# Kernel tuning notes

Measured on AMD Instinct MI355X. Metric: run time of the kernel, lower is better.

## Reference

```python
import jax, jax.numpy as jnp
import numpy as np

NUM_HEADS = 12
NUM_FRAMES = 8
WINDOW = (14, 14)


def _gen_relative_position_index(ws):
    h, w = ws
    num_rel = (2 * h - 1) * (2 * w - 1) + 3
    area = h * w
    coords = np.stack(np.meshgrid(np.arange(h), np.arange(w), indexing='ij'))  # (2,h,w)
    cf = coords.reshape(2, -1)
    rel = cf[:, :, None] - cf[:, None, :]  # (2,A,A)
    rel = rel.transpose(1, 2, 0).astype(np.int64)
    rel[:, :, 0] += h - 1
    rel[:, :, 1] += w - 1
    rel[:, :, 0] *= 2 * w - 1
    idx = np.zeros((area + 1, area + 1), dtype=np.int32)
    idx[1:, 1:] = rel.sum(-1)
    idx[0, :] = num_rel - 3
    idx[:, 0] = num_rel - 2
    idx[0, 0] = num_rel - 1
    return idx


def _gen_relative_temporal_index(nf):
    c = np.arange(nf)
    return (c[:, None] - c[None, :] + nf - 1).astype(np.int32)


def setup_inputs() -> dict:
    key = jax.random.key(0)
    ks = jax.random.split(key, 8)
    B, N, C = 2, NUM_FRAMES * WINDOW[0] * WINDOW[1], 768  # N = 1568
    num_rel = (2 * WINDOW[0] - 1) * (2 * WINDOW[1] - 1) + 3  # 732
    return {
        'x': jax.random.normal(ks[0], (B, N, C), jnp.float32),
        'qkv_w': jax.random.normal(ks[1], (3 * C, C), jnp.float32) * 0.02,
        'q_bias': jax.random.normal(ks[2], (C,), jnp.float32) * 0.02,
        'v_bias': jax.random.normal(ks[3], (C,), jnp.float32) * 0.02,
        'rel_pos_table': jax.random.normal(ks[4], (num_rel, NUM_HEADS), jnp.float32) * 0.02,
        'rel_temp_table': jax.random.normal(ks[5], (2 * NUM_FRAMES - 1, NUM_HEADS), jnp.float32) * 0.02,
        'proj_w': jax.random.normal(ks[6], (C, C), jnp.float32) * 0.02,
        'proj_b': jax.random.normal(ks[7], (C,), jnp.float32) * 0.02,
        'rel_pos_index': jnp.asarray(_gen_relative_position_index(WINDOW)),
        'rel_temp_index': jnp.asarray(_gen_relative_temporal_index(NUM_FRAMES)),
    }


def reference(x, qkv_w, q_bias, v_bias, rel_pos_table, rel_temp_table, proj_w, proj_b,
              rel_pos_index, rel_temp_index):
    B, N, C = x.shape
    H = NUM_HEADS
    D = C // H
    scale = D ** -0.5
    nf = NUM_FRAMES

    # qkv projection with concat(q_bias, zeros(k), v_bias)
    qkv_bias = jnp.concatenate([q_bias, jnp.zeros_like(q_bias), v_bias])
    qkv = x @ qkv_w.T + qkv_bias  # [B,N,3C]
    qkv = qkv.reshape(B, N, 3, H, D).transpose(2, 0, 3, 1, 4)  # [3,B,H,N,D]
    q, k, v = qkv[0], qkv[1], qkv[2]

    attn = jnp.einsum('bhqd,bhkd->bhqk', q * scale, k)  # [B,H,N,N]

    # gathered 2D relative position bias, tiled over frames, sliced to N
    rel = rel_pos_table[rel_pos_index]  # [197,197,H]
    rel = jnp.transpose(rel, (2, 0, 1))[None]  # [1,H,197,197]
    rel = jnp.tile(rel, (1, 1, nf, nf))[:, :, :N, :N]
    attn = attn + rel

    # temporal bias, repeat_interleave by tokens-per-frame
    tpf = N // nf  # 196
    temp = rel_temp_table[rel_temp_index]  # [nf,nf,H]
    temp = jnp.transpose(temp, (2, 0, 1))[None]  # [1,H,nf,nf]
    temp = jnp.repeat(jnp.repeat(temp, tpf, axis=2), tpf, axis=3)  # [1,H,N,N]
    attn = attn + temp

    attn = jax.nn.softmax(attn, axis=-1)
    attn = jnp.nan_to_num(attn, nan=0.0)

    out = jnp.einsum('bhqk,bhkd->bhqd', attn, v)  # [B,H,N,D]
    out = out.transpose(0, 2, 1, 3).reshape(B, N, C)
    return out @ proj_w.T + proj_b
```

## Files before the change

### kernel.cpp

```cpp
#include <hip/hip_runtime.h>
#include <hip/hip_bf16.h>

#define NHEADS 12
#define NFRAMES 8
#define NTOK 1568
#define CDIM 768
#define DHEAD 64
#define BATCH 2
#define MROWS (BATCH * NTOK)
#define MPAD 3200
#define K3 (3 * CDIM)
#define AREA1 197
#define TPF 196
#define LOG2E 1.4426950408889634f

typedef __bf16 bf16x8 __attribute__((ext_vector_type(8)));
typedef float f32x4 __attribute__((ext_vector_type(4)));
typedef float f32x16 __attribute__((ext_vector_type(16)));
typedef unsigned short u16x8 __attribute__((ext_vector_type(8)));

#if __has_builtin(__builtin_amdgcn_exp2f)
#define EXP2(x) __builtin_amdgcn_exp2f(x)
#else
#define EXP2(x) exp2f(x)
#endif

__device__ __forceinline__ unsigned short f2bf(float f) {
  return __builtin_bit_cast(unsigned short, (__bf16)f);
}
__device__ __forceinline__ float bf2f(unsigned short u) {
  unsigned int x = ((unsigned int)u) << 16;
  return __builtin_bit_cast(float, x);
}
__device__ __forceinline__ bf16x8 ld8(const unsigned short* p) {
  return __builtin_bit_cast(bf16x8, *(const u16x8*)p);
}
__device__ __forceinline__ f32x4 mfma16(bf16x8 a, bf16x8 b, f32x4 c) {
  return __builtin_amdgcn_mfma_f32_16x16x32_bf16(a, b, c, 0, 0, 0);
}
__device__ __forceinline__ f32x16 mfma32(bf16x8 a, bf16x8 b, f32x16 c) {
  return __builtin_amdgcn_mfma_f32_32x32x16_bf16(a, b, c, 0, 0, 0);
}
__device__ __forceinline__ unsigned int pack2(float lo, float hi) {
  return ((unsigned int)f2bf(hi) << 16) | (unsigned int)f2bf(lo);
}
__device__ __forceinline__ void swap32(unsigned int a, unsigned int b,
                                       unsigned int& x, unsigned int& y) {
#if __has_builtin(__builtin_amdgcn_permlane32_swap)
  auto r = __builtin_amdgcn_permlane32_swap(a, b, false, false);
  x = r[0]; y = r[1];
#else
  const bool hi = (threadIdx.x & 63) >= 32;
  unsigned int ea = (unsigned int)__shfl_xor((int)a, 32);
  unsigned int eb = (unsigned int)__shfl_xor((int)b, 32);
  x = hi ? eb : a;
  y = hi ? b : ea;
#endif
}
#define GL_LDS(src, dst)                                                    \
  __builtin_amdgcn_global_load_lds(                                         \
      (const __attribute__((address_space(1))) void*)(src),                 \
      (__attribute__((address_space(3))) void*)(dst), 16, 0, 0)

__device__ __forceinline__ int xcd_swz(int lin, int nwg) {
  const int q = nwg >> 3, r = nwg & 7;
  const int xcd = lin & 7, idx = lin >> 3;
  return (xcd < r ? xcd * (q + 1) : r * (q + 1) + (xcd - r) * q) + idx;
}

__global__ void biasP_kernel(const float* __restrict__ rpt,
                             const int* __restrict__ rpi,
                             const float* __restrict__ rtt,
                             const int* __restrict__ rti,
                             unsigned short* __restrict__ biasP,
                             float* __restrict__ bias2) {
  if (blockIdx.x == NHEADS * AREA1) {
    int t = threadIdx.x;
    for (; t < NHEADS * 64; t += 256) {
      int h = t >> 6, ff = t & 63;
      bias2[t] = rtt[rti[ff] * NHEADS + h] * LOG2E;
    }
    return;
  }
  __shared__ float row[AREA1];
  const int h = blockIdx.x / AREA1;
  const int i = blockIdx.x - h * AREA1;
  for (int j = threadIdx.x; j < AREA1; j += 256)
    row[j] = rpt[rpi[i * AREA1 + j] * NHEADS + h] * LOG2E;
  __syncthreads();
  unsigned short* dst = biasP + (size_t)blockIdx.x * 49 * 32;
  for (int e = threadIdx.x; e < 49 * 32; e += 256) {
    const int t = e >> 5, r = e & 31;
    const int hi = r >> 4, rr = r & 15;
    int km = 32 * t + (rr & 3) + 8 * (rr >> 2) + 4 * hi;
    km %= AREA1;
    dst[e] = f2bf(row[km]);
  }
}

template <int MODE, int BM, int BN, int TPB, int WAVES_M, int NB_N>
__global__ __launch_bounds__(TPB) void gemm_kernel(
    const float* __restrict__ Afp,
    const unsigned short* __restrict__ Abf,
    const float* __restrict__ Bfp,
    const float* __restrict__ bias0,
    const float* __restrict__ biasv,
    unsigned short* __restrict__ qbuf,
    unsigned short* __restrict__ kbuf,
    unsigned short* __restrict__ vtbuf,
    float* __restrict__ Cout) {
  constexpr int WAVES = TPB / 64;
  constexpr int WAVES_N = WAVES / WAVES_M;
  constexpr int WM = BM / WAVES_M;
  constexpr int WN = BN / WAVES_N;
  static_assert(BM * 4 == TPB && BN * 4 == TPB, "one chunk per thread");
  __shared__ unsigned short As[2][BM * 32];
  __shared__ unsigned short Bs[2][BN * 32];
  const int lane = threadIdx.x & 63;
  const int wv = threadIdx.x >> 6;
  const int tid = threadIdx.x;
  const int wg = xcd_swz(blockIdx.x, gridDim.x);
  const int m0 = (wg / NB_N) * BM;
  const int n0 = (wg % NB_N) * BN;

  const int srow = tid >> 2;
  const int srcc = (tid & 3) ^ ((tid >> 3) & 3);
  int arow = m0 + srow; if (arow >= MROWS) arow = MROWS - 1;
  const int brow = n0 + srow;

  f32x4 ra0, ra1, rb0, rb1;
  auto issueLoads = [&](int kt, int buf) {
    const int k0 = kt * 32 + srcc * 8;
    if (MODE == 0) {
      const f32x4* ap = (const f32x4*)(Afp + (size_t)arow * CDIM + k0);
      ra0 = ap[0]; ra1 = ap[1];
    } else {
      GL_LDS(Abf + (size_t)arow * CDIM + k0, &As[buf][tid * 8]);
    }
    const f32x4* bp = (const f32x4*)(Bfp + (size_t)brow * CDIM + k0);
    rb0 = bp[0]; rb1 = bp[1];
  };
  auto writeStage = [&](int buf) {
    u16x8 w;
    if (MODE == 0) {
      w[0] = f2bf(ra0[0]); w[1] = f2bf(ra0[1]); w[2] = f2bf(ra0[2]);
      w[3] = f2bf(ra0[3]); w[4] = f2bf(ra1[0]); w[5] = f2bf(ra1[1]);
      w[6] = f2bf(ra1[2]); w[7] = f2bf(ra1[3]);
      *(u16x8*)&As[buf][tid * 8] = w;
    }
    w[0] = f2bf(rb0[0]); w[1] = f2bf(rb0[1]); w[2] = f2bf(rb0[2]);
    w[3] = f2bf(rb0[3]); w[4] = f2bf(rb1[0]); w[5] = f2bf(rb1[1]);
    w[6] = f2bf(rb1[2]); w[7] = f2bf(rb1[3]);
    *(u16x8*)&Bs[buf][tid * 8] = w;
  };

  f32x4 acc[WM / 16][WN / 16] = {};
  const int rbase = (wv & (WAVES_M - 1)) * WM;
  const int cbase = (wv / WAVES_M) * WN;
  const int lc = lane >> 4;

  issueLoads(0, 0);
  __builtin_amdgcn_sched_barrier(0);
  writeStage(0);
  __syncthreads();
  int cur = 0;
  for (int kt = 0; kt < CDIM / 32; ++kt) {
    if (kt + 1 < CDIM / 32) issueLoads(kt + 1, cur ^ 1);
    __builtin_amdgcn_sched_barrier(0);
    bf16x8 af[WM / 16], bg[WN / 16];
#pragma unroll
    for (int i = 0; i < WM / 16; ++i) {
      const int ra = rbase + i * 16 + (lane & 15);
      af[i] = ld8(&As[cur][ra * 32 + ((lc ^ ((ra >> 1) & 3)) << 3)]);
    }
#pragma unroll
    for (int j = 0; j < WN / 16; ++j) {
      const int rb = cbase + j * 16 + (lane & 15);
      bg[j] = ld8(&Bs[cur][rb * 32 + ((lc ^ ((rb >> 1) & 3)) << 3)]);
    }
#pragma unroll
    for (int i = 0; i < WM / 16; ++i)
#pragma unroll
      for (int j = 0; j < WN / 16; ++j)
        acc[i][j] = mfma16(af[i], bg[j], acc[i][j]);
    if (kt + 1 < CDIM / 32) writeStage(cur ^ 1);
    __syncthreads();
    cur ^= 1;
  }

#pragma unroll
  for (int i = 0; i < WM / 16; ++i) {
#pragma unroll
    for (int j = 0; j < WN / 16; ++j) {
#pragma unroll
      for (int r = 0; r < 4; ++r) {
        int grow = m0 + rbase + i * 16 + (lane >> 4) * 4 + r;
        int gcol = n0 + cbase + j * 16 + (lane & 15);
        if (grow >= MROWS) continue;
        float v = acc[i][j][r];
        if (MODE == 0) {
          int which = gcol / CDIM;
          int cc = gcol - which * CDIM;
          int hh = cc >> 6, dd = cc & 63;
          int b = grow / NTOK, n = grow - b * NTOK;
          size_t hd = ((size_t)(b * NHEADS + hh) * NTOK + n) * 64 + dd;
          if (which == 0)
            qbuf[hd] = f2bf((v + bias0[cc]) * (0.125f * LOG2E));
          else if (which == 1)
            kbuf[hd] = f2bf(v);
          else
            vtbuf[((size_t)(b * NHEADS + hh) * 64 + dd) * NTOK + n] =
                f2bf(v + biasv[cc]);
        } else {
          Cout[(size_t)grow * CDIM + gcol] = v + bias0[gcol];
        }
      }
    }
  }
}

__global__ __launch_bounds__(256) void attn_kernel(
    const unsigned short* __restrict__ qbuf,
    const unsigned short* __restrict__ kbuf,
    const unsigned short* __restrict__ vtbuf,
    const unsigned short* __restrict__ biasP,
    const float* __restrict__ bias2,
    unsigned short* __restrict__ aout) {
  __shared__ __align__(16) char smem[36864];
  unsigned short* stg = (unsigned short*)smem;
  float* mb = (float*)smem;

  const int lane = threadIdx.x & 63;
  const int wv = threadIdx.x >> 6;
  const int wu = (blockIdx.x & 7) * 147 + (blockIdx.x >> 3);
  const int bh = wu / 49;
  const int qt = wu - bh * 49;
  const int q0 = qt * 32;
  const int h = bh % NHEADS;
  const int b = bh / NHEADS;
  const int qlane = lane & 31;
  const int hi = lane >> 5;
  const int hi4 = hi * 4;
  const int qn = q0 + qlane;
  const int qfr = qn / TPF < 7 ? qn / TPF : 7;
  const int qmod = qn % AREA1;

  const unsigned short* qp = qbuf + (size_t)bh * NTOK * DHEAD;
  const unsigned short* kp = kbuf + (size_t)bh * NTOK * DHEAD;
  const unsigned short* vp = vtbuf + (size_t)bh * DHEAD * NTOK;
  const unsigned short* bP = biasP + ((size_t)(h * AREA1 + qmod) * 49) * 32 + hi * 16;
  const float* b2q = bias2 + h * 64 + qfr * 8;

  unsigned short* KsW = stg + wv * 4096;
  unsigned short* VsW = KsW + 2048;

  const unsigned short* ksb =
      kp + (size_t)(lane >> 3) * DHEAD + (((lane & 7) ^ (lane >> 3)) << 3);
  const unsigned short* vsb =
      vp + (size_t)(lane >> 2) * NTOK + (((lane & 3) ^ ((lane >> 3) & 3)) << 3);

  auto stage = [&](int gt) {
    const int kv0 = gt * 32;
#pragma unroll
    for (int j = 0; j < 4; ++j) {
      GL_LDS(ksb + (size_t)(kv0 + j * 8) * DHEAD, KsW + j * 512);
      GL_LDS(vsb + kv0 + (size_t)(j * 16) * NTOK, VsW + j * 512);
    }
  };

  bf16x8 aq[4];
#pragma unroll
  for (int c = 0; c < 4; ++c)
    aq[c] = ld8(qp + (size_t)qn * DHEAD + c * 16 + hi * 8);

  f32x16 o0 = {}, o1 = {};
  float lrun = 0.f;

  stage(wv);
  u16x8 ubA, ubB;
  {
    const u16x8* bp = (const u16x8*)(bP + (size_t)wv * 32);
    ubA = bp[0]; ubB = bp[1];
  }
  int kfl = 0;
  float b2lo = b2q[0], b2hi = b2q[1];
  const int skey = qlane & 7;
  const int vswz = (qlane >> 1) & 3;

  for (int gt = wv; gt < 49; gt += 4) {
    asm volatile("s_waitcnt vmcnt(0)" ::: "memory");
    __builtin_amdgcn_sched_barrier(0);
    bf16x8 kf[4];
#pragma unroll
    for (int c = 0; c < 4; ++c)
      kf[c] = ld8(&KsW[qlane * 64 + ((((c << 1) + hi) ^ skey) << 3)]);
    bf16x8 vf0 = ld8(&VsW[qlane * 32 + ((hi ^ vswz) << 3)]);
    bf16x8 vf1 = ld8(&VsW[qlane * 32 + (((2 + hi) ^ vswz) << 3)]);
    bf16x8 vf2 = ld8(&VsW[(32 + qlane) * 32 + ((hi ^ vswz) << 3)]);
    bf16x8 vf3 = ld8(&VsW[(32 + qlane) * 32 + (((2 + hi) ^ vswz) << 3)]);
    asm volatile("s_waitcnt lgkmcnt(0)" ::: "memory");
    __builtin_amdgcn_sched_barrier(0);
    const bool more = (gt + 4 < 49);
    if (more) stage(gt + 4);

    f32x16 s;
#pragma unroll
    for (int r = 0; r < 16; ++r)
      s[r] = ((r < 8) ? bf2f(ubA[r]) : bf2f(ubB[r - 8])) + b2lo;
    __builtin_amdgcn_s_setprio(1);
#pragma unroll
    for (int c = 0; c < 4; ++c) s = mfma32(kf[c], aq[c], s);
    __builtin_amdgcn_s_setprio(0);

    const int ccr = (kfl + 1) * TPF - gt * 32;
    int kfln = kfl;
    float nb2lo = b2lo, nb2hi = b2hi;
    if (more) {
      const u16x8* bp = (const u16x8*)(bP + (size_t)(gt + 4) * 32);
      ubA = bp[0]; ubB = bp[1];
      kfln = ((gt + 4) * 8) / 49;
      nb2lo = b2q[kfln];
      nb2hi = b2q[kfln < 7 ? kfln + 1 : 7];
    }

    if (ccr < 32) {
      const float dlt = b2hi - b2lo;
#pragma unroll
      for (int r = 0; r < 16; ++r)
        s[r] += ((r & 3) + 8 * (r >> 2) + hi4 >= ccr) ? dlt : 0.f;
    }

#pragma unroll
    for (int r = 0; r < 16; ++r) s[r] = EXP2(s[r]);
    float ps;
    {
      float a = (s[0] + s[1]) + (s[2] + s[3]);
      float bb = (s[4] + s[5]) + (s[6] + s[7]);
      float cc = (s[8] + s[9]) + (s[10] + s[11]);
      float dd = (s[12] + s[13]) + (s[14] + s[15]);
      ps = (a + bb) + (cc + dd);
    }
    {
      unsigned int px, py;
      swap32(__builtin_bit_cast(unsigned int, ps),
             __builtin_bit_cast(unsigned int, ps), px, py);
      ps = __builtin_bit_cast(float, px) + __builtin_bit_cast(float, py);
    }
    lrun += ps;

    unsigned int dw[8];
#pragma unroll
    for (int c = 0; c < 8; ++c) dw[c] = pack2(s[2 * c], s[2 * c + 1]);
    unsigned int f0[4], f1[4];
    swap32(dw[0], dw[2], f0[0], f0[2]);
    swap32(dw[1], dw[3], f0[1], f0[3]);
    swap32(dw[4], dw[6], f1[0], f1[2]);
    swap32(dw[5], dw[7], f1[1], f1[3]);
    const bf16x8 F0 = __builtin_bit_cast(bf16x8, *(ulonglong2*)f0);
    const bf16x8 F1 = __builtin_bit_cast(bf16x8, *(ulonglong2*)f1);

    __builtin_amdgcn_s_setprio(1);
    o0 = mfma32(vf0, F0, o0);
    o0 = mfma32(vf1, F1, o0);
    o1 = mfma32(vf2, F0, o1);
    o1 = mfma32(vf3, F1, o1);
    __builtin_amdgcn_s_setprio(0);

    kfl = kfln;
    b2lo = nb2lo;
    b2hi = nb2hi;
  }

  __syncthreads();
  float* mrow = mb + (size_t)(wv * 64 + lane) * 34;
#pragma unroll
  for (int r = 0; r < 16; ++r) {
    mrow[r] = o0[r];
    mrow[16 + r] = o1[r];
  }
  mrow[32] = lrun;
  __syncthreads();
  if (wv < 2) {
    const int off = wv * 16;
    float acc[16];
#pragma unroll
    for (int r = 0; r < 16; ++r) acc[r] = 0.f;
    float L = 0.f;
#pragma unroll
    for (int w2 = 0; w2 < 4; ++w2) {
      const float* rr = mb + (size_t)(w2 * 64 + lane) * 34;
      L += rr[32];
#pragma unroll
      for (int r = 0; r < 16; ++r) acc[r] += rr[off + r];
    }
    const float rinv = 1.0f / L;
    unsigned short* op = aout + (size_t)(b * NTOK + qn) * CDIM + h * 64 + wv * 32;
#pragma unroll
    for (int c = 0; c < 8; ++c) {
      const int d0 = 8 * (c >> 1) + 4 * hi + 2 * (c & 1);
      *(unsigned int*)(op + d0) = pack2(acc[2 * c] * rinv, acc[2 * c + 1] * rinv);
    }
  }
}

extern "C" void kernel_launch(void* const* d_in, const int* in_sizes, int n_in,
                              void* d_out, int out_size, void* d_ws, size_t ws_size,
                              hipStream_t stream) {
  (void)in_sizes; (void)n_in; (void)out_size; (void)ws_size;
  const float* x        = (const float*)d_in[0];
  const float* qkv_w    = (const float*)d_in[1];
  const float* q_bias   = (const float*)d_in[2];
  const float* v_bias   = (const float*)d_in[3];
  const float* rp_table = (const float*)d_in[4];
  const float* rt_table = (const float*)d_in[5];
  const float* proj_w   = (const float*)d_in[6];
  const float* proj_b   = (const float*)d_in[7];
  const int* rp_index   = (const int*)d_in[8];
  const int* rt_index   = (const int*)d_in[9];

  char* ws = (char*)d_ws;
  unsigned short* qbuf   = (unsigned short*)(ws + 9633792);
  unsigned short* kbuf   = (unsigned short*)(ws + 14450688);
  unsigned short* vtbuf  = (unsigned short*)(ws + 19267584);
  unsigned short* aout   = (unsigned short*)(ws + 24084480);
  unsigned short* biasP  = (unsigned short*)(ws);
  float* bias2           = (float*)(ws + 30247424);

  gemm_kernel<0, 128, 128, 512, 4, K3 / 128>
      <<<dim3((K3 / 128) * (MPAD / 128)), 512, 0, stream>>>(
          x, nullptr, qkv_w, q_bias, v_bias, qbuf, kbuf, vtbuf, nullptr);
  biasP_kernel<<<NHEADS * AREA1 + 1, 256, 0, stream>>>(
      rp_table, rp_index, rt_table, rt_index, biasP, bias2);
  attn_kernel<<<dim3(1176), 256, 0, stream>>>(
      qbuf, kbuf, vtbuf, biasP, bias2, aout);
  gemm_kernel<1, 64, 64, 256, 2, CDIM / 64>
      <<<dim3((CDIM / 64) * (MPAD / 64)), 256, 0, stream>>>(
          nullptr, aout, proj_w, proj_b, nullptr, nullptr, nullptr, nullptr,
          (float*)d_out);
}
```

Before: 113.6 us.

## Fuse relative-bias table build into a dedicated QKV projection GEMM kernel

```diff
diff --git a/kernel.cpp b/kernel.cpp
--- a/kernel.cpp
+++ b/kernel.cpp
@@ -68,33 +68,148 @@
   return (xcd < r ? xcd * (q + 1) : r * (q + 1) + (xcd - r) * q) + idx;
 }
 
-__global__ void biasP_kernel(const float* __restrict__ rpt,
-                             const int* __restrict__ rpi,
-                             const float* __restrict__ rtt,
-                             const int* __restrict__ rti,
-                             unsigned short* __restrict__ biasP,
-                             float* __restrict__ bias2) {
-  if (blockIdx.x == NHEADS * AREA1) {
-    int t = threadIdx.x;
-    for (; t < NHEADS * 64; t += 256) {
-      int h = t >> 6, ff = t & 63;
-      bias2[t] = rtt[rti[ff] * NHEADS + h] * LOG2E;
+__global__ __launch_bounds__(512) void gemm0_kernel(
+    const float* __restrict__ x,
+    const float* __restrict__ qkv_w,
+    const float* __restrict__ q_bias,
+    const float* __restrict__ v_bias,
+    unsigned short* __restrict__ qbuf,
+    unsigned short* __restrict__ kbuf,
+    unsigned short* __restrict__ vtbuf,
+    const float* __restrict__ rpt,
+    const int* __restrict__ rpi,
+    const float* __restrict__ rtt,
+    const int* __restrict__ rti,
+    unsigned short* __restrict__ biasP,
+    float* __restrict__ bias2) {
+  __shared__ __align__(16) char smem[65536];
+  unsigned short* As = (unsigned short*)smem;
+  unsigned short* Bs = As + 16384;
+
+  if (blockIdx.x >= 450) {
+    const int bb = blockIdx.x - 450;
+    if (bb == NHEADS * AREA1) {
+      for (int t = threadIdx.x; t < NHEADS * 64; t += 512) {
+        int h = t >> 6, ff = t & 63;
+        bias2[t] = rtt[rti[ff] * NHEADS + h] * LOG2E;
+      }
+      return;
+    }
+    float* row = (float*)smem;
+    const int h = bb / AREA1;
+    const int i = bb - h * AREA1;
+    for (int j = threadIdx.x; j < AREA1; j += 512)
+      row[j] = rpt[rpi[i * AREA1 + j] * NHEADS + h] * LOG2E;
+    __syncthreads();
+    unsigned short* dst = biasP + (size_t)bb * 49 * 32;
+    for (int e = threadIdx.x; e < 49 * 32; e += 512) {
+      const int t = e >> 5, r = e & 31;
+      const int hi = r >> 4, rr = r & 15;
+      int km = 32 * t + (rr & 3) + 8 * (rr >> 2) + 4 * hi;
+      km %= AREA1;
+      dst[e] = f2bf(row[km]);
     }
     return;
   }
-  __shared__ float row[AREA1];
-  const int h = blockIdx.x / AREA1;
-  const int i = blockIdx.x - h * AREA1;
-  for (int j = threadIdx.x; j < AREA1; j += 256)
-    row[j] = rpt[rpi[i * AREA1 + j] * NHEADS + h] * LOG2E;
+
+  const int lane = threadIdx.x & 63;
+  const int wv = threadIdx.x >> 6;
+  const int tid = threadIdx.x;
+  const int wg = xcd_swz(blockIdx.x, 450);
+  const int m0 = (wg / 18) * 128;
+  const int n0 = (wg % 18) * 128;
+
+  const int srow = tid >> 3;
+  const int srcc = (tid & 7) ^ ((tid >> 3) & 7);
+  int ar0 = m0 + srow;      if (ar0 >= MROWS) ar0 = MROWS - 1;
+  int ar1 = m0 + 64 + srow; if (ar1 >= MROWS) ar1 = MROWS - 1;
+  const int br0 = n0 + srow, br1 = n0 + 64 + srow;
+
+  f32x4 ra[4], rb[4];
+  auto issueLoads = [&](int kt) {
+    const int k0 = kt * 64 + srcc * 8;
+    const f32x4* p;
+    p = (const f32x4*)(x + (size_t)ar0 * CDIM + k0);     ra[0] = p[0]; ra[1] = p[1];
+    p = (const f32x4*)(x + (size_t)ar1 * CDIM + k0);     ra[2] = p[0]; ra[3] = p[1];
+    p = (const f32x4*)(qkv_w + (size_t)br0 * CDIM + k0); rb[0] = p[0]; rb[1] = p[1];
+    p = (const f32x4*)(qkv_w + (size_t)br1 * CDIM + k0); rb[2] = p[0]; rb[3] = p[1];
+  };
+  auto cvt8 = [&](const f32x4& a, const f32x4& b) {
+    u16x8 w;
+    w[0] = f2bf(a[0]); w[1] = f2bf(a[1]); w[2] = f2bf(a[2]); w[3] = f2bf(a[3]);
+    w[4] = f2bf(b[0]); w[5] = f2bf(b[1]); w[6] = f2bf(b[2]); w[7] = f2bf(b[3]);
+    return w;
+  };
+  auto writeStage = [&](int buf) {
+    const int o = buf * 8192 + (tid >> 3) * 64 + (tid & 7) * 8;
+    *(u16x8*)&As[o]        = cvt8(ra[0], ra[1]);
+    *(u16x8*)&As[o + 4096] = cvt8(ra[2], ra[3]);
+    *(u16x8*)&Bs[o]        = cvt8(rb[0], rb[1]);
+    *(u16x8*)&Bs[o + 4096] = cvt8(rb[2], rb[3]);
+  };
+
+  f32x4 acc[2][4] = {};
+  const int rbase = (wv & 3) * 32;
+  const int cbase = (wv >> 2) * 64;
+  const int lc = lane >> 4;
+
+  issueLoads(0);
+  __builtin_amdgcn_sched_barrier(0);
+  writeStage(0);
   __syncthreads();
-  unsigned short* dst = biasP + (size_t)blockIdx.x * 49 * 32;
-  for (int e = threadIdx.x; e < 49 * 32; e += 256) {
-    const int t = e >> 5, r = e & 31;
-    const int hi = r >> 4, rr = r & 15;
-    int km = 32 * t + (rr & 3) + 8 * (rr >> 2) + 4 * hi;
-    km %= AREA1;
-    dst[e] = f2bf(row[km]);
+  int cur = 0;
+  for (int kt = 0; kt < CDIM / 64; ++kt) {
+    if (kt + 1 < CDIM / 64) issueLoads(kt + 1);
+    __builtin_amdgcn_sched_barrier(0);
+#pragma unroll
+    for (int s = 0; s < 2; ++s) {
+      const int c = s * 4 + lc;
+      bf16x8 af[2], bg[4];
+#pragma unroll
+      for (int i = 0; i < 2; ++i) {
+        const int rr = rbase + i * 16 + (lane & 15);
+        af[i] = ld8(&As[cur * 8192 + rr * 64 + ((c ^ (rr & 7)) << 3)]);
+      }
+#pragma unroll
+      for (int j = 0; j < 4; ++j) {
+        const int rr = cbase + j * 16 + (lane & 15);
+        bg[j] = ld8(&Bs[cur * 8192 + rr * 64 + ((c ^ (rr & 7)) << 3)]);
+      }
+#pragma unroll
+      for (int i = 0; i < 2; ++i)
+#pragma unroll
+        for (int j = 0; j < 4; ++j)
+          acc[i][j] = mfma16(af[i], bg[j], acc[i][j]);
+    }
+    if (kt + 1 < CDIM / 64) writeStage(cur ^ 1);
+    __syncthreads();
+    cur ^= 1;
+  }
+
+#pragma unroll
+  for (int i = 0; i < 2; ++i) {
+#pragma unroll
+    for (int j = 0; j < 4; ++j) {
+#pragma unroll
+      for (int r = 0; r < 4; ++r) {
+        int grow = m0 + rbase + i * 16 + (lane >> 4) * 4 + r;
+        int gcol = n0 + cbase + j * 16 + (lane & 15);
+        if (grow >= MROWS) continue;
+        float v = acc[i][j][r];
+        int which = gcol / CDIM;
+        int cc = gcol - which * CDIM;
+        int hh = cc >> 6, dd = cc & 63;
+        int b = grow / NTOK, n = grow - b * NTOK;
+        size_t hd = ((size_t)(b * NHEADS + hh) * NTOK + n) * 64 + dd;
+        if (which == 0)
+          qbuf[hd] = f2bf((v + q_bias[cc]) * (0.125f * LOG2E));
+        else if (which == 1)
+          kbuf[hd] = f2bf(v);
+        else
+          vtbuf[((size_t)(b * NHEADS + hh) * 64 + dd) * NTOK + n] =
+              f2bf(v + v_bias[cc]);
+      }
+    }
   }
 }
 
@@ -426,10 +541,8 @@
   unsigned short* biasP  = (unsigned short*)(ws);
   float* bias2           = (float*)(ws + 30247424);
 
-  gemm_kernel<0, 128, 128, 512, 4, K3 / 128>
-      <<<dim3((K3 / 128) * (MPAD / 128)), 512, 0, stream>>>(
-          x, nullptr, qkv_w, q_bias, v_bias, qbuf, kbuf, vtbuf, nullptr);
-  biasP_kernel<<<NHEADS * AREA1 + 1, 256, 0, stream>>>(
+  gemm0_kernel<<<dim3(450 + NHEADS * AREA1 + 1), 512, 0, stream>>>(
+      x, qkv_w, q_bias, v_bias, qbuf, kbuf, vtbuf,
       rp_table, rp_index, rt_table, rt_index, biasP, bias2);
   attn_kernel<<<dim3(1176), 256, 0, stream>>>(
       qbuf, kbuf, vtbuf, biasP, bias2, aout);
```

Result: faster. 106.2 us (-6.5%).
